# Optimization experiments

Measured on AMD Instinct MI355X. Metric: run time of the kernel, lower is better.

## Reference

```python
import jax, jax.numpy as jnp
import numpy as np

B, N, DIM, IN_DIM, H = 8, 3136, 147, 64, 1
HD = IN_DIM // H          # per-head value/key dim = 64
MLP_HID = int(IN_DIM * 1.0)
EPS = 1e-5


def _ln(x, w, b):
    m = jnp.mean(x, axis=-1, keepdims=True)
    v = jnp.mean((x - m) ** 2, axis=-1, keepdims=True)
    return (x - m) / jnp.sqrt(v + EPS) * w + b


def setup_inputs() -> dict:
    key = jax.random.key(0)
    ks = jax.random.split(key, 12)
    r = lambda k, shp, s=0.02: (jax.random.normal(k, shp, dtype=jnp.float32) * s)
    return {
        "x": jax.random.normal(ks[0], (B, N, DIM), dtype=jnp.float32),
        "norm1_w": jnp.ones((DIM,), jnp.float32),
        "norm1_b": jnp.zeros((DIM,), jnp.float32),
        "qkv_w": r(ks[1], (3 * IN_DIM, DIM)),
        "scale": jnp.full((H,), (DIM // H) ** -0.5, dtype=jnp.float32),
        "proj_w": r(ks[2], (IN_DIM, IN_DIM)),
        "proj_b": jnp.zeros((IN_DIM,), jnp.float32),
        "norm2_w": jnp.ones((IN_DIM,), jnp.float32),
        "norm2_b": jnp.zeros((IN_DIM,), jnp.float32),
        "fc1_w": r(ks[3], (MLP_HID, IN_DIM)),
        "fc1_b": jnp.zeros((MLP_HID,), jnp.float32),
        "fc2_w": r(ks[4], (IN_DIM, MLP_HID)),
        "fc2_b": jnp.zeros((IN_DIM,), jnp.float32),
    }


def reference(x, norm1_w, norm1_b, qkv_w, scale, proj_w, proj_b,
              norm2_w, norm2_b, fc1_w, fc1_b, fc2_w, fc2_b):
    h = _ln(x, norm1_w, norm1_b)                               # [B,N,DIM]
    qkv = jnp.einsum('bnc,oc->bno', h, qkv_w)                  # [B,N,3*IN_DIM]
    qkv = qkv.reshape(B, N, 3, H, HD).transpose(2, 0, 3, 1, 4)  # [3,B,H,N,HD]
    q, k, v = qkv[0], qkv[1], qkv[2]
    # LMSA: learnable per-head scale + diagonal (self) exclusion mask
    attn = jnp.einsum('bhid,bhjd->bhij', q, k) * scale[None, :, None, None]
    eye = jnp.eye(N, dtype=bool)
    attn = jnp.where(eye[None, None], -jnp.inf, attn)
    attn = jax.nn.softmax(attn, axis=-1)
    o = jnp.einsum('bhij,bhjd->bhid', attn, v)                 # [B,H,N,HD]
    o = o.transpose(0, 2, 1, 3).reshape(B, N, IN_DIM)
    o = jnp.einsum('bnd,od->bno', o, proj_w) + proj_b
    # num_heads == 1 -> residual is v itself
    x_attn = v[:, 0] + o                                       # [B,N,IN_DIM]
    h2 = _ln(x_attn, norm2_w, norm2_b)
    h2 = jax.nn.gelu(jnp.einsum('bnd,hd->bnh', h2, fc1_w) + fc1_b,
                     approximate=False)
    h2 = jnp.einsum('bnh,oh->bno', h2, fc2_w) + fc2_b
    return x_attn + h2
```

## Files before the change

### kernel.cpp

```cpp
#include <hip/hip_runtime.h>
#include <math.h>
#include <stdint.h>

#define B_    8
#define N_    3136
#define DIM_  147
#define KP_   160
#define TOK_  (B_*N_)
#define QKV3_ 192

typedef __attribute__((ext_vector_type(4))) float f32x4;
typedef __attribute__((ext_vector_type(4))) unsigned int u32x4;
typedef __attribute__((ext_vector_type(8))) short short8;
typedef union { short8 s; u32x4 u; } pk8;

static __device__ __forceinline__ unsigned short f2b(float f){
  unsigned int u = __float_as_uint(f);
  u += 0x7fffu + ((u>>16)&1u);
  return (unsigned short)(u>>16);
}
static __device__ __forceinline__ unsigned int pk2(float a, float b){
  return ((unsigned int)f2b(b)<<16) | (unsigned int)f2b(a);
}
static __device__ __forceinline__ unsigned int pk2t(float a, float b){
  return (__float_as_uint(b) & 0xffff0000u) | (__float_as_uint(a)>>16);
}
static __device__ __forceinline__ float b2f(unsigned short s){
  return __uint_as_float(((unsigned int)s)<<16);
}

#define GLD16(gp, lp) __builtin_amdgcn_global_load_lds( \
    reinterpret_cast<const uint32_t __attribute__((address_space(1)))*>(reinterpret_cast<uintptr_t>(gp)), \
    reinterpret_cast<uint32_t __attribute__((address_space(3)))*>(reinterpret_cast<uintptr_t>(lp)), \
    16, 0, 0)

__global__ __launch_bounds__(256) void k_prep(const float* __restrict__ qkvw,
                                              const float* __restrict__ projw,
                                              const float* __restrict__ fc1w,
                                              const float* __restrict__ fc2w,
                                              unsigned short* __restrict__ wp,
                                              unsigned short* __restrict__ wpj,
                                              unsigned short* __restrict__ w1b,
                                              unsigned short* __restrict__ w2b){
  int idx = blockIdx.x*256 + threadIdx.x;
  if(idx < QKV3_*KP_){
    int n = idx / KP_, k = idx - n*KP_;
    wp[idx] = f2b((k < DIM_) ? qkvw[n*DIM_ + k] : 0.f);
  }
  if(idx < 4096){
    wpj[idx] = f2b(projw[idx]);
    w1b[idx] = f2b(fc1w[idx]);
    w2b[idx] = f2b(fc2w[idx]);
  }
}

__global__ __launch_bounds__(256,2) void k_qkv(const float* __restrict__ x,
                                               const float* __restrict__ w1,
                                               const float* __restrict__ b1,
                                               const unsigned short* __restrict__ wp,
                                               const float* __restrict__ scale,
                                               unsigned short* __restrict__ qb,
                                               unsigned short* __restrict__ kb,
                                               unsigned short* __restrict__ vtb,
                                               unsigned short* __restrict__ vfb){
  __shared__ alignas(16) unsigned short A_[32*168];
  __shared__ alignas(16) unsigned short VT[64*36];
  int tid = threadIdx.x;
  int w = tid>>6, lane = tid&63, quad = lane>>4, l16 = lane&15;
  int t0 = blockIdx.x*32;
  float sc2 = scale[0] * 1.44269504089f;

  {
    int g = tid>>3, e = tid&7;
    const float* xr = x + (size_t)(t0+g)*147;
    float xv[19];
    float s = 0.f, sq = 0.f;
    #pragma unroll
    for(int i=0;i<19;i++){
      int col = e + 8*i;
      float v = (col < 147) ? xr[col] : 0.f;
      xv[i] = v; s += v; sq += v*v;
    }
    s  += __shfl_xor(s,1,64);  s  += __shfl_xor(s,2,64);  s  += __shfl_xor(s,4,64);
    sq += __shfl_xor(sq,1,64); sq += __shfl_xor(sq,2,64); sq += __shfl_xor(sq,4,64);
    float mean = s*(1.f/147.f);
    float var  = sq*(1.f/147.f) - mean*mean;
    float rstd = rsqrtf(var + 1e-5f);
    #pragma unroll
    for(int i=0;i<19;i++){
      int col = e + 8*i;
      if(col < 147) A_[g*168 + col] = f2b((xv[i]-mean)*rstd*w1[col] + b1[col]);
    }
    #pragma unroll
    for(int i=0;i<2;i++){
      int col = 144 + e + 8*i;
      if(col >= 147 && col < 160) A_[g*168 + col] = 0;
    }
  }
  __syncthreads();
  int mh = (w&1)*16, cb = (w>>1)*96;
  short8 Af[5];
  #pragma unroll
  for(int kk=0;kk<5;kk++)
    Af[kk] = *(const short8*)(A_ + (mh+l16)*168 + kk*32 + quad*8);
  f32x4 acc[6];
  #pragma unroll
  for(int i=0;i<6;i++) acc[i] = (f32x4){0.f,0.f,0.f,0.f};
  #pragma unroll
  for(int nt=0;nt<6;nt++){
    #pragma unroll
    for(int kk=0;kk<5;kk++){
      short8 Bf = *(const short8*)(wp + (size_t)(cb+nt*16+l16)*160 + kk*32 + quad*8);
      acc[nt] = __builtin_amdgcn_mfma_f32_16x16x32_bf16(Af[kk], Bf, acc[nt], 0,0,0);
    }
  }
  #pragma unroll
  for(int nt=0;nt<6;nt++){
    int o = cb + nt*16 + l16;
    #pragma unroll
    for(int r=0;r<4;r++){
      int tl = mh + quad*4 + r;
      int mg = t0 + tl;
      float val = acc[nt][r];
      if(o < 64){
        qb[(size_t)mg*64 + o] = f2b(val*sc2);
      } else if(o < 128){
        kb[(size_t)mg*64 + (o-64)] = f2b(val);
      } else {
        int hd = o - 128;
        unsigned short vb = f2b(val);
        vfb[(size_t)mg*64 + hd] = vb;
        VT[hd*36 + tl] = vb;
      }
    }
  }
  __syncthreads();
  {
    int b = t0 / N_, n0 = t0 - b*N_;
    const unsigned int* VT32 = (const unsigned int*)VT;
    unsigned int* vg = (unsigned int*)vtb + ((size_t)b*64)*(N_/2) + (n0>>1);
    for(int rep=0;rep<4;rep++){
      int f = rep*256 + tid;
      int row = f>>4, c = f&15;
      vg[(size_t)row*(N_/2) + c] = VT32[row*18 + c];
    }
  }
}

__global__ __launch_bounds__(128,4) void k_attn(const unsigned short* __restrict__ qb,
                                                const unsigned short* __restrict__ kb,
                                                const unsigned short* __restrict__ vtb,
                                                unsigned short* __restrict__ Opart,
                                                float* __restrict__ lpart){
  __shared__ alignas(16) unsigned int L[4096];
  unsigned int* Ks = L;
  unsigned int* Vs = L + 2048;
  int tid = threadIdx.x;
  int w = tid>>6, lane = tid&63, quad = lane>>4, l16 = lane&15;
  int qt = blockIdx.x, sp = blockIdx.y, b = blockIdx.z;
  int kv0 = (sp*49)>>2, kv1 = ((sp+1)*49)>>2;

  short8 Qf[2][2];
  {
    const unsigned short* qg = qb + ((size_t)b*N_ + qt*64 + w*32)*64;
    #pragma unroll
    for(int qs=0;qs<2;qs++)
      #pragma unroll
      for(int kk=0;kk<2;kk++)
        Qf[qs][kk] = *(const short8*)(qg + (qs*16+l16)*64 + kk*32 + quad*8);
  }
  int koffL[4], voffL[4];
  {
    int pl = lane>>3, cl = lane&7;
    #pragma unroll
    for(int rr=0;rr<4;rr++){
      int p = w*32 + rr*8 + pl;
      int sig = (p&32)|((p&12)<<1)|((p&16)>>2)|(p&3);
      int cx = cl ^ (p&7);
      koffL[rr] = sig*128 + cx*16;
      voffL[rr] = p*(N_*2) + cx*16;
    }
  }
  const char* kBase = (const char*)kb + (size_t)b*N_*128;
  const char* vBase = (const char*)vtb + (size_t)b*64*(size_t)(N_*2);

  f32x4 O[2][4];
  #pragma unroll
  for(int qs=0;qs<2;qs++) for(int j=0;j<4;j++) O[qs][j] = (f32x4){0.f,0.f,0.f,0.f};
  float lr[2] = {0.f, 0.f};
  const unsigned short* Ksh = (const unsigned short*)Ks;
  const unsigned short* Vsh = (const unsigned short*)Vs;
  int r7 = l16&7;
  int ku0 = (quad ^ r7)*8;
  int ku1 = ((4+quad) ^ r7)*8;
  int dloc = w*32 + l16;

  for(int kvt=kv0; kvt<kv1; ++kvt){
    __syncthreads();
    {
      const char* kT = kBase + (size_t)kvt*8192;
      const char* vT = vBase + (size_t)kvt*128;
      #pragma unroll
      for(int rr=0;rr<4;rr++){
        GLD16(kT + koffL[rr], (char*)Ks + (w*32+rr*8)*128);
        GLD16(vT + voffL[rr], (char*)Vs + (w*32+rr*8)*128);
      }
    }
    __syncthreads();

    pk8 Pb[2][2];
    #pragma unroll
    for(int qs=0;qs<2;qs++){
      f32x4 S[4];
      #pragma unroll
      for(int jt=0;jt<4;jt++){
        short8 Kf0 = *(const short8*)(Ksh + jt*1024 + l16*64 + ku0);
        short8 Kf1 = *(const short8*)(Ksh + jt*1024 + l16*64 + ku1);
        f32x4 z = (f32x4){0.f,0.f,0.f,0.f};
        S[jt] = __builtin_amdgcn_mfma_f32_16x16x32_bf16(Kf0, Qf[qs][0], z, 0,0,0);
        S[jt] = __builtin_amdgcn_mfma_f32_16x16x32_bf16(Kf1, Qf[qs][1], S[jt], 0,0,0);
      }
      float p[4][4];
      if(kvt == qt){
        int dl = dloc + qs*16;
        #pragma unroll
        for(int jt=0;jt<4;jt++){
          int kvb = (jt>>1)*32 + (jt&1)*4 + quad*8;
          #pragma unroll
          for(int r=0;r<4;r++){
            float pv = (kvb + r == dl) ? 0.f : __builtin_amdgcn_exp2f(S[jt][r]);
            p[jt][r] = pv; lr[qs] += pv;
          }
        }
      } else {
        #pragma unroll
        for(int jt=0;jt<4;jt++)
          #pragma unroll
          for(int r=0;r<4;r++){
            float pv = __builtin_amdgcn_exp2f(S[jt][r]);
            p[jt][r] = pv; lr[qs] += pv;
          }
      }
      Pb[qs][0].u = (u32x4){ pk2t(p[0][0],p[0][1]), pk2t(p[0][2],p[0][3]),
                             pk2t(p[1][0],p[1][1]), pk2t(p[1][2],p[1][3]) };
      Pb[qs][1].u = (u32x4){ pk2t(p[2][0],p[2][1]), pk2t(p[2][2],p[2][3]),
                             pk2t(p[3][0],p[3][1]), pk2t(p[3][2],p[3][3]) };
    }
    #pragma unroll
    for(int jt2=0;jt2<4;jt2++){
      short8 Vf0 = *(const short8*)(Vsh + jt2*1024 + l16*64 + ku0);
      short8 Vf1 = *(const short8*)(Vsh + jt2*1024 + l16*64 + ku1);
      O[0][jt2] = __builtin_amdgcn_mfma_f32_16x16x32_bf16(Vf0, Pb[0][0].s, O[0][jt2], 0,0,0);
      O[0][jt2] = __builtin_amdgcn_mfma_f32_16x16x32_bf16(Vf1, Pb[0][1].s, O[0][jt2], 0,0,0);
      O[1][jt2] = __builtin_amdgcn_mfma_f32_16x16x32_bf16(Vf0, Pb[1][0].s, O[1][jt2], 0,0,0);
      O[1][jt2] = __builtin_amdgcn_mfma_f32_16x16x32_bf16(Vf1, Pb[1][1].s, O[1][jt2], 0,0,0);
    }
  }
  lr[0] += __shfl_xor(lr[0],16,64); lr[0] += __shfl_xor(lr[0],32,64);
  lr[1] += __shfl_xor(lr[1],16,64); lr[1] += __shfl_xor(lr[1],32,64);
  __syncthreads();
  #pragma unroll
  for(int qs=0;qs<2;qs++){
    int q = w*32 + qs*16 + l16;
    #pragma unroll
    for(int jt2=0;jt2<4;jt2++){
      L[q*36 + jt2*8 + quad*2]     = pk2(O[qs][jt2][0], O[qs][jt2][1]);
      L[q*36 + jt2*8 + quad*2 + 1] = pk2(O[qs][jt2][2], O[qs][jt2][3]);
    }
  }
  if(quad == 0){
    size_t lbase = (size_t)sp*TOK_ + (size_t)b*N_ + qt*64 + w*32;
    lpart[lbase + l16]      = lr[0];
    lpart[lbase + 16 + l16] = lr[1];
  }
  __syncthreads();
  {
    unsigned int* og = (unsigned int*)(Opart + ((size_t)sp*TOK_ + (size_t)b*N_ + qt*64)*64);
    for(int rep=0;rep<4;rep++){
      int f = rep*128 + tid;
      int row = f>>3, c = f&7;
      *(u32x4*)(og + row*32 + c*4) = *(const u32x4*)&L[row*36 + c*4];
    }
  }
}

__global__ __launch_bounds__(128) void k_mlp(const unsigned short* __restrict__ Opart,
                                             const float* __restrict__ lpart,
                                             const unsigned short* __restrict__ vfb,
                                             const unsigned short* __restrict__ wpj,
                                             const unsigned short* __restrict__ w1b,
                                             const unsigned short* __restrict__ w2b,
                                             const float* __restrict__ projb,
                                             const float* __restrict__ n2w,
                                             const float* __restrict__ n2b,
                                             const float* __restrict__ fc1b,
                                             const float* __restrict__ fc2b,
                                             float* __restrict__ out){
  __shared__ alignas(16) unsigned short Xs[32*72];
  unsigned int* Xs32 = (unsigned int*)Xs;
  int tid = threadIdx.x;
  int w = tid>>6, lane = tid&63, quad = lane>>4, l16 = lane&15;
  int t0 = blockIdx.x*32;

  #pragma unroll
  for(int i=0;i<2;i++){
    int f = i*128 + tid;
    int row = f>>3, c = f&7;
    float lo[4] = {0,0,0,0}, hi[4] = {0,0,0,0};
    float lsum = 0.f;
    #pragma unroll
    for(int s=0;s<4;s++){
      u32x4 a = *((const u32x4*)(Opart + ((size_t)s*TOK_ + t0)*64) + row*8 + c);
      #pragma unroll
      for(int k=0;k<4;k++){
        lo[k] += __uint_as_float(a[k]<<16);
        hi[k] += __uint_as_float(a[k] & 0xffff0000u);
      }
      lsum += lpart[(size_t)s*TOK_ + t0 + row];
    }
    float linv = 1.f/lsum;
    u32x4 o;
    #pragma unroll
    for(int k=0;k<4;k++) o[k] = pk2(lo[k]*linv, hi[k]*linv);
    *(u32x4*)&Xs32[row*36 + c*4] = o;
  }
  __syncthreads();

  short8 Af[2];
  #pragma unroll
  for(int kk=0;kk<2;kk++)
    Af[kk] = *(const short8*)(Xs + (w*16+l16)*72 + kk*32 + quad*8);
  f32x4 acc[4];
  #pragma unroll
  for(int i=0;i<4;i++) acc[i] = (f32x4){0.f,0.f,0.f,0.f};
  #pragma unroll
  for(int jt=0;jt<4;jt++)
    #pragma unroll
    for(int kk=0;kk<2;kk++){
      short8 Bf = *(const short8*)(wpj + (jt*16+l16)*64 + kk*32 + quad*8);
      acc[jt] = __builtin_amdgcn_mfma_f32_16x16x32_bf16(Af[kk], Bf, acc[jt], 0,0,0);
    }
  float xa[4][4];
  #pragma unroll
  for(int jt=0;jt<4;jt++){
    int col = jt*16 + l16;
    float pb = projb[col];
    #pragma unroll
    for(int r=0;r<4;r++){
      int tg = t0 + w*16 + quad*4 + r;
      xa[jt][r] = acc[jt][r] + pb + b2f(vfb[(size_t)tg*64 + col]);
    }
  }
  #pragma unroll
  for(int r=0;r<4;r++){
    float s = 0.f, sq = 0.f;
    #pragma unroll
    for(int jt=0;jt<4;jt++){ s += xa[jt][r]; sq += xa[jt][r]*xa[jt][r]; }
    s  += __shfl_xor(s,1,64);  s  += __shfl_xor(s,2,64);
    s  += __shfl_xor(s,4,64);  s  += __shfl_xor(s,8,64);
    sq += __shfl_xor(sq,1,64); sq += __shfl_xor(sq,2,64);
    sq += __shfl_xor(sq,4,64); sq += __shfl_xor(sq,8,64);
    float mu = s*(1.f/64.f);
    float var = sq*(1.f/64.f) - mu*mu;
    float rstd = rsqrtf(var + 1e-5f);
    #pragma unroll
    for(int jt=0;jt<4;jt++){
      int col = jt*16 + l16;
      Xs[(w*16+quad*4+r)*72 + col] = f2b((xa[jt][r]-mu)*rstd*n2w[col] + n2b[col]);
    }
  }
  #pragma unroll
  for(int kk=0;kk<2;kk++)
    Af[kk] = *(const short8*)(Xs + (w*16+l16)*72 + kk*32 + quad*8);
  f32x4 acc2[4];
  #pragma unroll
  for(int i=0;i<4;i++) acc2[i] = (f32x4){0.f,0.f,0.f,0.f};
  #pragma unroll
  for(int jt=0;jt<4;jt++)
    #pragma unroll
    for(int kk=0;kk<2;kk++){
      short8 Bf = *(const short8*)(w1b + (jt*16+l16)*64 + kk*32 + quad*8);
      acc2[jt] = __builtin_amdgcn_mfma_f32_16x16x32_bf16(Af[kk], Bf, acc2[jt], 0,0,0);
    }
  #pragma unroll
  for(int jt=0;jt<4;jt++){
    int col = jt*16 + l16;
    float fb = fc1b[col];
    #pragma unroll
    for(int r=0;r<4;r++){
      float g = acc2[jt][r] + fb;
      float z = g*0.70710678118f;
      float az = fabsf(z);
      float t = 1.f/(1.f + 0.3275911f*az);
      float poly = ((((1.061405429f*t - 1.453152027f)*t + 1.421413741f)*t - 0.284496736f)*t + 0.254829592f)*t;
      float er = 1.f - poly*__builtin_amdgcn_exp2f(-az*az*1.44269504089f);
      er = (z < 0.f) ? -er : er;
      Xs[(w*16+quad*4+r)*72 + col] = f2b(0.5f*g*(1.f + er));
    }
  }
  #pragma unroll
  for(int kk=0;kk<2;kk++)
    Af[kk] = *(const short8*)(Xs + (w*16+l16)*72 + kk*32 + quad*8);
  f32x4 acc3[4];
  #pragma unroll
  for(int i=0;i<4;i++) acc3[i] = (f32x4){0.f,0.f,0.f,0.f};
  #pragma unroll
  for(int jt=0;jt<4;jt++)
    #pragma unroll
    for(int kk=0;kk<2;kk++){
      short8 Bf = *(const short8*)(w2b + (jt*16+l16)*64 + kk*32 + quad*8);
      acc3[jt] = __builtin_amdgcn_mfma_f32_16x16x32_bf16(Af[kk], Bf, acc3[jt], 0,0,0);
    }
  #pragma unroll
  for(int jt=0;jt<4;jt++){
    int col = jt*16 + l16;
    float ob2 = fc2b[col];
    #pragma unroll
    for(int r=0;r<4;r++){
      int tg = t0 + w*16 + quad*4 + r;
      out[(size_t)tg*64 + col] = xa[jt][r] + acc3[jt][r] + ob2;
    }
  }
}

extern "C" void kernel_launch(void* const* d_in, const int* in_sizes, int n_in,
                              void* d_out, int out_size, void* d_ws, size_t ws_size,
                              hipStream_t stream){
  const float* x     = (const float*)d_in[0];
  const float* n1w   = (const float*)d_in[1];
  const float* n1b   = (const float*)d_in[2];
  const float* qkvw  = (const float*)d_in[3];
  const float* scale = (const float*)d_in[4];
  const float* projw = (const float*)d_in[5];
  const float* projb = (const float*)d_in[6];
  const float* n2w   = (const float*)d_in[7];
  const float* n2b   = (const float*)d_in[8];
  const float* fc1w  = (const float*)d_in[9];
  const float* fc1b  = (const float*)d_in[10];
  const float* fc2w  = (const float*)d_in[11];
  const float* fc2b  = (const float*)d_in[12];

  char* base = (char*)d_ws;
  unsigned short* wp  = (unsigned short*)(base + 0);
  unsigned short* wpj = (unsigned short*)(base + 61440);
  unsigned short* w1b = (unsigned short*)(base + 69632);
  unsigned short* w2b = (unsigned short*)(base + 77824);
  unsigned short* qb  = (unsigned short*)(base + 86016);
  unsigned short* kb  = (unsigned short*)(base + 3297280);
  unsigned short* vtb = (unsigned short*)(base + 6508544);
  unsigned short* vfb = (unsigned short*)(base + 9719808);
  unsigned short* Op  = (unsigned short*)(base + 12931072);
  float*          lp  = (float*)(base + 25776128);

  hipLaunchKernelGGL(k_prep, dim3(120),      dim3(256), 0, stream,
                     qkvw, projw, fc1w, fc2w, wp, wpj, w1b, w2b);
  hipLaunchKernelGGL(k_qkv,  dim3(TOK_/32),  dim3(256), 0, stream,
                     x, n1w, n1b, wp, scale, qb, kb, vtb, vfb);
  hipLaunchKernelGGL(k_attn, dim3(49,4,8),   dim3(128), 0, stream, qb, kb, vtb, Op, lp);
  hipLaunchKernelGGL(k_mlp,  dim3(TOK_/32),  dim3(128), 0, stream, Op, lp, vfb,
                     wpj, w1b, w2b, projb, n2w, n2b, fc1b, fc2b, (float*)d_out);
}
```

Before: 154.2 us.

## Stage weights in LDS, double tile sizes, and batch two KV tiles per sync

New measurement: 145.8 us. 1.06x faster.

```diff
diff --git a/kernel.cpp b/kernel.cpp
--- a/kernel.cpp
+++ b/kernel.cpp
@@ -8,10 +8,11 @@
 #define KP_   160
 #define TOK_  (B_*N_)
 #define QKV3_ 192
-
-typedef __attribute__((ext_vector_type(4))) float f32x4;
-typedef __attribute__((ext_vector_type(4))) unsigned int u32x4;
-typedef __attribute__((ext_vector_type(8))) short short8;
+#define NSPLIT 4
+
+typedef __attribute__((ext_vector_type(4)))  float f32x4;
+typedef __attribute__((ext_vector_type(4)))  unsigned int u32x4;
+typedef __attribute__((ext_vector_type(8)))  short short8;
 typedef union { short8 s; u32x4 u; } pk8;
 
 static __device__ __forceinline__ unsigned short f2b(float f){
@@ -54,24 +55,26 @@
   }
 }
 
-__global__ __launch_bounds__(256,2) void k_qkv(const float* __restrict__ x,
-                                               const float* __restrict__ w1,
-                                               const float* __restrict__ b1,
-                                               const unsigned short* __restrict__ wp,
-                                               const float* __restrict__ scale,
-                                               unsigned short* __restrict__ qb,
-                                               unsigned short* __restrict__ kb,
-                                               unsigned short* __restrict__ vtb,
-                                               unsigned short* __restrict__ vfb){
-  __shared__ alignas(16) unsigned short A_[32*168];
-  __shared__ alignas(16) unsigned short VT[64*36];
+__global__ __launch_bounds__(256) void k_qkv(const float* __restrict__ x,
+                                             const float* __restrict__ w1,
+                                             const float* __restrict__ b1,
+                                             const unsigned short* __restrict__ wp,
+                                             const float* __restrict__ scale,
+                                             unsigned short* __restrict__ qb,
+                                             unsigned short* __restrict__ kb,
+                                             unsigned short* __restrict__ vtb,
+                                             unsigned short* __restrict__ vfb){
+  __shared__ alignas(16) unsigned short Wb[192*168];
+  unsigned short* A_ = Wb;
+  unsigned short* VT = Wb;
   int tid = threadIdx.x;
   int w = tid>>6, lane = tid&63, quad = lane>>4, l16 = lane&15;
-  int t0 = blockIdx.x*32;
+  int t0 = blockIdx.x*64;
   float sc2 = scale[0] * 1.44269504089f;
 
-  {
-    int g = tid>>3, e = tid&7;
+  #pragma unroll
+  for(int half=0; half<2; half++){
+    int g = half*32 + (tid>>3), e = tid&7;
     const float* xr = x + (size_t)(t0+g)*147;
     float xv[19];
     float s = 0.f, sq = 0.f;
@@ -98,51 +101,64 @@
     }
   }
   __syncthreads();
-  int mh = (w&1)*16, cb = (w>>1)*96;
   short8 Af[5];
   #pragma unroll
   for(int kk=0;kk<5;kk++)
-    Af[kk] = *(const short8*)(A_ + (mh+l16)*168 + kk*32 + quad*8);
-  f32x4 acc[6];
-  #pragma unroll
-  for(int i=0;i<6;i++) acc[i] = (f32x4){0.f,0.f,0.f,0.f};
-  #pragma unroll
-  for(int nt=0;nt<6;nt++){
+    Af[kk] = *(const short8*)(A_ + (w*16+l16)*168 + kk*32 + quad*8);
+  __syncthreads();
+  {
+    const u32x4* src = (const u32x4*)wp;
+    unsigned int* dst = (unsigned int*)Wb;
+    #pragma unroll
+    for(int rep=0; rep<15; rep++){
+      int idx = rep*256 + tid;
+      int row = idx/20, c = idx - row*20;
+      *(u32x4*)(dst + row*84 + c*4) = src[idx];
+    }
+  }
+  __syncthreads();
+  f32x4 acc[12];
+  #pragma unroll
+  for(int i=0;i<12;i++) acc[i] = (f32x4){0.f,0.f,0.f,0.f};
+  #pragma unroll
+  for(int nt=0;nt<12;nt++){
     #pragma unroll
     for(int kk=0;kk<5;kk++){
-      short8 Bf = *(const short8*)(wp + (size_t)(cb+nt*16+l16)*160 + kk*32 + quad*8);
+      short8 Bf = *(const short8*)(Wb + (nt*16+l16)*168 + kk*32 + quad*8);
       acc[nt] = __builtin_amdgcn_mfma_f32_16x16x32_bf16(Af[kk], Bf, acc[nt], 0,0,0);
     }
   }
   #pragma unroll
-  for(int nt=0;nt<6;nt++){
-    int o = cb + nt*16 + l16;
+  for(int nt=0;nt<12;nt++){
+    int o = nt*16 + l16;
     #pragma unroll
     for(int r=0;r<4;r++){
-      int tl = mh + quad*4 + r;
+      int tl = w*16 + quad*4 + r;
       int mg = t0 + tl;
       float val = acc[nt][r];
-      if(o < 64){
-        qb[(size_t)mg*64 + o] = f2b(val*sc2);
-      } else if(o < 128){
-        kb[(size_t)mg*64 + (o-64)] = f2b(val);
-      } else {
-        int hd = o - 128;
-        unsigned short vb = f2b(val);
-        vfb[(size_t)mg*64 + hd] = vb;
-        VT[hd*36 + tl] = vb;
-      }
-    }
+      if(o < 64)        qb[(size_t)mg*64 + o]        = f2b(val*sc2);
+      else if(o < 128)  kb[(size_t)mg*64 + (o-64)]   = f2b(val);
+      else              vfb[(size_t)mg*64 + (o-128)] = f2b(val);
+    }
+  }
+  __syncthreads();
+  #pragma unroll
+  for(int nt=8;nt<12;nt++){
+    int hd = (nt-8)*16 + l16;
+    #pragma unroll
+    for(int r=0;r<4;r++)
+      VT[hd*72 + (w*16 + quad*4 + r)] = f2b(acc[nt][r]);
   }
   __syncthreads();
   {
     int b = t0 / N_, n0 = t0 - b*N_;
     const unsigned int* VT32 = (const unsigned int*)VT;
     unsigned int* vg = (unsigned int*)vtb + ((size_t)b*64)*(N_/2) + (n0>>1);
-    for(int rep=0;rep<4;rep++){
+    #pragma unroll
+    for(int rep=0;rep<8;rep++){
       int f = rep*256 + tid;
-      int row = f>>4, c = f&15;
-      vg[(size_t)row*(N_/2) + c] = VT32[row*18 + c];
+      int row = f>>5, c = f&31;
+      vg[(size_t)row*(N_/2) + c] = VT32[row*36 + c];
     }
   }
 }
@@ -152,9 +168,7 @@
                                                 const unsigned short* __restrict__ vtb,
                                                 unsigned short* __restrict__ Opart,
                                                 float* __restrict__ lpart){
-  __shared__ alignas(16) unsigned int L[4096];
-  unsigned int* Ks = L;
-  unsigned int* Vs = L + 2048;
+  __shared__ alignas(16) unsigned int L[2][4096];
   int tid = threadIdx.x;
   int w = tid>>6, lane = tid&63, quad = lane>>4, l16 = lane&15;
   int qt = blockIdx.x, sp = blockIdx.y, b = blockIdx.z;
@@ -188,26 +202,23 @@
   #pragma unroll
   for(int qs=0;qs<2;qs++) for(int j=0;j<4;j++) O[qs][j] = (f32x4){0.f,0.f,0.f,0.f};
   float lr[2] = {0.f, 0.f};
-  const unsigned short* Ksh = (const unsigned short*)Ks;
-  const unsigned short* Vsh = (const unsigned short*)Vs;
   int r7 = l16&7;
   int ku0 = (quad ^ r7)*8;
   int ku1 = ((4+quad) ^ r7)*8;
   int dloc = w*32 + l16;
 
-  for(int kvt=kv0; kvt<kv1; ++kvt){
-    __syncthreads();
-    {
-      const char* kT = kBase + (size_t)kvt*8192;
-      const char* vT = vBase + (size_t)kvt*128;
-      #pragma unroll
-      for(int rr=0;rr<4;rr++){
-        GLD16(kT + koffL[rr], (char*)Ks + (w*32+rr*8)*128);
-        GLD16(vT + voffL[rr], (char*)Vs + (w*32+rr*8)*128);
-      }
-    }
-    __syncthreads();
-
+  auto stage = [&](unsigned int* buf, int kvt){
+    const char* kT = kBase + (size_t)kvt*8192;
+    const char* vT = vBase + (size_t)kvt*128;
+    #pragma unroll
+    for(int rr=0;rr<4;rr++){
+      GLD16(kT + koffL[rr], (char*)buf + (w*32+rr*8)*128);
+      GLD16(vT + voffL[rr], (char*)buf + 8192 + (w*32+rr*8)*128);
+    }
+  };
+  auto compute = [&](const unsigned int* buf, int t){
+    const unsigned short* Ksh = (const unsigned short*)buf;
+    const unsigned short* Vsh = (const unsigned short*)(buf + 2048);
     pk8 Pb[2][2];
     #pragma unroll
     for(int qs=0;qs<2;qs++){
@@ -221,7 +232,7 @@
         S[jt] = __builtin_amdgcn_mfma_f32_16x16x32_bf16(Kf1, Qf[qs][1], S[jt], 0,0,0);
       }
       float p[4][4];
-      if(kvt == qt){
+      if(t == qt){
         int dl = dloc + qs*16;
         #pragma unroll
         for(int jt=0;jt<4;jt++){
@@ -255,17 +266,29 @@
       O[1][jt2] = __builtin_amdgcn_mfma_f32_16x16x32_bf16(Vf0, Pb[1][0].s, O[1][jt2], 0,0,0);
       O[1][jt2] = __builtin_amdgcn_mfma_f32_16x16x32_bf16(Vf1, Pb[1][1].s, O[1][jt2], 0,0,0);
     }
-  }
+  };
+
+  for(int tt=kv0; tt<kv1; tt+=2){
+    bool two = (tt+1 < kv1);
+    __syncthreads();
+    stage(L[0], tt);
+    if(two) stage(L[1], tt+1);
+    __syncthreads();
+    compute(L[0], tt);
+    if(two) compute(L[1], tt+1);
+  }
+
   lr[0] += __shfl_xor(lr[0],16,64); lr[0] += __shfl_xor(lr[0],32,64);
   lr[1] += __shfl_xor(lr[1],16,64); lr[1] += __shfl_xor(lr[1],32,64);
   __syncthreads();
+  unsigned int* Ls = &L[0][0];
   #pragma unroll
   for(int qs=0;qs<2;qs++){
     int q = w*32 + qs*16 + l16;
     #pragma unroll
     for(int jt2=0;jt2<4;jt2++){
-      L[q*36 + jt2*8 + quad*2]     = pk2(O[qs][jt2][0], O[qs][jt2][1]);
-      L[q*36 + jt2*8 + quad*2 + 1] = pk2(O[qs][jt2][2], O[qs][jt2][3]);
+      Ls[q*36 + jt2*8 + quad*2]     = pk2(O[qs][jt2][0], O[qs][jt2][1]);
+      Ls[q*36 + jt2*8 + quad*2 + 1] = pk2(O[qs][jt2][2], O[qs][jt2][3]);
     }
   }
   if(quad == 0){
@@ -276,15 +299,16 @@
   __syncthreads();
   {
     unsigned int* og = (unsigned int*)(Opart + ((size_t)sp*TOK_ + (size_t)b*N_ + qt*64)*64);
+    #pragma unroll
     for(int rep=0;rep<4;rep++){
       int f = rep*128 + tid;
       int row = f>>3, c = f&7;
-      *(u32x4*)(og + row*32 + c*4) = *(const u32x4*)&L[row*36 + c*4];
-    }
-  }
-}
-
-__global__ __launch_bounds__(128) void k_mlp(const unsigned short* __restrict__ Opart,
+      *(u32x4*)(og + row*32 + c*4) = *(const u32x4*)&Ls[row*36 + c*4];
+    }
+  }
+}
+
+__global__ __launch_bounds__(256) void k_mlp(const unsigned short* __restrict__ Opart,
                                              const float* __restrict__ lpart,
                                              const unsigned short* __restrict__ vfb,
                                              const unsigned short* __restrict__ wpj,
@@ -296,20 +320,31 @@
                                              const float* __restrict__ fc1b,
                                              const float* __restrict__ fc2b,
                                              float* __restrict__ out){
-  __shared__ alignas(16) unsigned short Xs[32*72];
+  __shared__ alignas(16) unsigned short Ws[3][64*72];
+  __shared__ alignas(16) unsigned short Xs[64*72];
   unsigned int* Xs32 = (unsigned int*)Xs;
   int tid = threadIdx.x;
   int w = tid>>6, lane = tid&63, quad = lane>>4, l16 = lane&15;
-  int t0 = blockIdx.x*32;
-
+  int t0 = blockIdx.x*64;
+
+  {
+    #pragma unroll
+    for(int rep=0;rep<2;rep++){
+      int f = rep*256 + tid;
+      int row = f>>3, c = f&7;
+      *(u32x4*)((unsigned int*)Ws[0] + row*36 + c*4) = ((const u32x4*)wpj)[row*8+c];
+      *(u32x4*)((unsigned int*)Ws[1] + row*36 + c*4) = ((const u32x4*)w1b)[row*8+c];
+      *(u32x4*)((unsigned int*)Ws[2] + row*36 + c*4) = ((const u32x4*)w2b)[row*8+c];
+    }
+  }
   #pragma unroll
   for(int i=0;i<2;i++){
-    int f = i*128 + tid;
+    int f = i*256 + tid;
     int row = f>>3, c = f&7;
     float lo[4] = {0,0,0,0}, hi[4] = {0,0,0,0};
     float lsum = 0.f;
     #pragma unroll
-    for(int s=0;s<4;s++){
+    for(int s=0;s<NSPLIT;s++){
       u32x4 a = *((const u32x4*)(Opart + ((size_t)s*TOK_ + t0)*64) + row*8 + c);
       #pragma unroll
       for(int k=0;k<4;k++){
@@ -337,7 +372,7 @@
   for(int jt=0;jt<4;jt++)
     #pragma unroll
     for(int kk=0;kk<2;kk++){
-      short8 Bf = *(const short8*)(wpj + (jt*16+l16)*64 + kk*32 + quad*8);
+      short8 Bf = *(const short8*)(Ws[0] + (jt*16+l16)*72 + kk*32 + quad*8);
       acc[jt] = __builtin_amdgcn_mfma_f32_16x16x32_bf16(Af[kk], Bf, acc[jt], 0,0,0);
     }
   float xa[4][4];
@@ -379,7 +414,7 @@
   for(int jt=0;jt<4;jt++)
     #pragma unroll
     for(int kk=0;kk<2;kk++){
-      short8 Bf = *(const short8*)(w1b + (jt*16+l16)*64 + kk*32 + quad*8);
+      short8 Bf = *(const short8*)(Ws[1] + (jt*16+l16)*72 + kk*32 + quad*8);
       acc2[jt] = __builtin_amdgcn_mfma_f32_16x16x32_bf16(Af[kk], Bf, acc2[jt], 0,0,0);
     }
   #pragma unroll
@@ -408,7 +443,7 @@
   for(int jt=0;jt<4;jt++)
     #pragma unroll
     for(int kk=0;kk<2;kk++){
-      short8 Bf = *(const short8*)(w2b + (jt*16+l16)*64 + kk*32 + quad*8);
+      short8 Bf = *(const short8*)(Ws[2] + (jt*16+l16)*72 + kk*32 + quad*8);
       acc3[jt] = __builtin_amdgcn_mfma_f32_16x16x32_bf16(Af[kk], Bf, acc3[jt], 0,0,0);
     }
   #pragma unroll
@@ -452,11 +487,11 @@
   unsigned short* Op  = (unsigned short*)(base + 12931072);
   float*          lp  = (float*)(base + 25776128);
 
-  hipLaunchKernelGGL(k_prep, dim3(120),      dim3(256), 0, stream,
+  hipLaunchKernelGGL(k_prep, dim3(120),        dim3(256), 0, stream,
                      qkvw, projw, fc1w, fc2w, wp, wpj, w1b, w2b);
-  hipLaunchKernelGGL(k_qkv,  dim3(TOK_/32),  dim3(256), 0, stream,
+  hipLaunchKernelGGL(k_qkv,  dim3(TOK_/64),    dim3(256), 0, stream,
                      x, n1w, n1b, wp, scale, qb, kb, vtb, vfb);
-  hipLaunchKernelGGL(k_attn, dim3(49,4,8),   dim3(128), 0, stream, qb, kb, vtb, Op, lp);
-  hipLaunchKernelGGL(k_mlp,  dim3(TOK_/32),  dim3(128), 0, stream, Op, lp, vfb,
+  hipLaunchKernelGGL(k_attn, dim3(49,NSPLIT,8), dim3(128), 0, stream, qb, kb, vtb, Op, lp);
+  hipLaunchKernelGGL(k_mlp,  dim3(TOK_/64),    dim3(256), 0, stream, Op, lp, vfb,
                      wpj, w1b, w2b, projb, n2w, n2b, fc1b, fc2b, (float*)d_out);
 }
```
